# Kernel tuning notes

Measured on AMD Instinct MI355X. Metric: run time of the kernel, lower is better.

Reference implementation:

```python
import jax, jax.numpy as jnp
import numpy as np

N = 50000      # nodes
H = 128        # hidden_size
RBF = 20       # edge_embedding_size
E_CHE = 400000 # chemical edges
E_VDW = 200000 # van-der-Waals edges


def _prelu(x, a):
    return jnp.where(x > 0, x, a * x)


def _mlp(x, w1, b1, a1, w2, b2, a2):
    # Linear -> PReLU -> Linear -> PReLU (PaiNN message / filter MLP)
    h = _prelu(x @ w1 + b1, a1)
    return _prelu(h @ w2 + b2, a2)


def setup_inputs() -> dict:
    key = jax.random.key(0)
    ks = list(jax.random.split(key, 64))
    it = iter(ks)
    d = {}
    d['node_scalar'] = jax.random.normal(next(it), (N, H), jnp.float32)
    d['node_vector'] = jax.random.normal(next(it), (N, 3, H), jnp.float32)
    for pfx, E in (('che', E_CHE), ('vdw', E_VDW)):
        d[pfx + '_edge'] = jax.random.randint(next(it), (E, 2), 0, N)
        d[pfx + '_edge_diff'] = jax.random.normal(next(it), (E, 3), jnp.float32)
        d[pfx + '_edge_dist'] = jax.random.uniform(next(it), (E,), jnp.float32) + 0.5  # strictly positive
        d[pfx + '_rbf_dist'] = jax.random.normal(next(it), (E, RBF), jnp.float32)
    # four 2-layer MLPs with per-layer PReLU scalar slope (torch default init 0.25)
    def mlp_params(pfx, din):
        s1 = 1.0 / np.sqrt(din)
        s2 = 1.0 / np.sqrt(H)
        d[pfx + '_w1'] = jax.random.uniform(next(it), (din, H), jnp.float32, -s1, s1)
        d[pfx + '_b1'] = jax.random.uniform(next(it), (H,), jnp.float32, -s1, s1)
        d[pfx + '_a1'] = jnp.asarray(0.25, jnp.float32)
        d[pfx + '_w2'] = jax.random.uniform(next(it), (H, 3 * H), jnp.float32, -s2, s2)
        d[pfx + '_b2'] = jax.random.uniform(next(it), (3 * H,), jnp.float32, -s2, s2)
        d[pfx + '_a2'] = jnp.asarray(0.25, jnp.float32)
    mlp_params('che_s', H)    # che scalar message MLP
    mlp_params('che_f', RBF)  # che filter layer
    mlp_params('vdw_s', H)
    mlp_params('vdw_f', RBF)
    return d


def _branch(node_scalar, node_vector, edge, edge_diff, edge_dist, rbf, sp, fp):
    # sp/fp: 6-tuples of MLP params. edge[:,1]=source gather, edge[:,0]=dest scatter.
    scalar_out = _mlp(node_scalar, *sp)          # [N, 3H]
    filter_w = _mlp(rbf, *fp)                    # [E, 3H]
    filter_out = scalar_out[edge[:, 1]] * filter_w  # gather + gate
    gate_vector, message_scalar, gate_edge = jnp.split(filter_out, 3, axis=1)
    state_vector = node_vector[edge[:, 1]] * gate_vector[:, None, :]        # [E,3,H]
    unit = edge_diff / edge_dist[:, None]                                    # [E,3]
    edge_vector = unit[:, :, None] * gate_edge[:, None, :]                   # [E,3,H]
    message_vector = state_vector + edge_vector
    res_scalar = jax.ops.segment_sum(message_scalar, edge[:, 0], num_segments=N)
    res_vector = jax.ops.segment_sum(message_vector, edge[:, 0], num_segments=N)
    return res_scalar, res_vector


def reference(node_scalar, node_vector,
              che_edge, che_edge_diff, che_edge_dist, che_rbf_dist,
              vdw_edge, vdw_edge_diff, vdw_edge_dist, vdw_rbf_dist,
              che_s_w1, che_s_b1, che_s_a1, che_s_w2, che_s_b2, che_s_a2,
              che_f_w1, che_f_b1, che_f_a1, che_f_w2, che_f_b2, che_f_a2,
              vdw_s_w1, vdw_s_b1, vdw_s_a1, vdw_s_w2, vdw_s_b2, vdw_s_a2,
              vdw_f_w1, vdw_f_b1, vdw_f_a1, vdw_f_w2, vdw_f_b2, vdw_f_a2):
    che_sp = (che_s_w1, che_s_b1, che_s_a1, che_s_w2, che_s_b2, che_s_a2)
    che_fp = (che_f_w1, che_f_b1, che_f_a1, che_f_w2, che_f_b2, che_f_a2)
    vdw_sp = (vdw_s_w1, vdw_s_b1, vdw_s_a1, vdw_s_w2, vdw_s_b2, vdw_s_a2)
    vdw_fp = (vdw_f_w1, vdw_f_b1, vdw_f_a1, vdw_f_w2, vdw_f_b2, vdw_f_a2)
    che_rs, che_rv = _branch(node_scalar, node_vector, che_edge, che_edge_diff,
                             che_edge_dist, che_rbf_dist, che_sp, che_fp)
    vdw_rs, vdw_rv = _branch(node_scalar, node_vector, vdw_edge, vdw_edge_diff,
                             vdw_edge_dist, vdw_rbf_dist, vdw_sp, vdw_fp)
    return (node_scalar + che_rs + vdw_rs, node_vector + che_rv + vdw_rv)
```

## Files before the change

### kernel.cpp

```cpp
#include <hip/hip_runtime.h>
#include <hip/hip_bf16.h>

typedef float f32x4 __attribute__((ext_vector_type(4)));
typedef short bf16x8 __attribute__((ext_vector_type(8)));

#define HD 128
#define TILE 32
#define SCAN_TILE 2048

__device__ __forceinline__ float prelu_f(float x, float a) {
  return x > 0.f ? x : a * x;
}

__device__ __forceinline__ unsigned short f2bf(float x) {
  __hip_bfloat16 h = __float2bfloat16(x);
  return *reinterpret_cast<unsigned short*>(&h);
}
__device__ __forceinline__ float bf2f(unsigned short u) {
  union { unsigned u; float f; } a; a.u = ((unsigned)u) << 16;
  return a.f;
}
__device__ __forceinline__ f32x4 bf4_to_f32(ushort4 u) {
  f32x4 r; r[0] = bf2f(u.x); r[1] = bf2f(u.y); r[2] = bf2f(u.z); r[3] = bf2f(u.w);
  return r;
}

__global__ __launch_bounds__(256) void init_conv_kernel(
    const f32x4* __restrict__ ns, const f32x4* __restrict__ nv,
    f32x4* __restrict__ out, ushort4* __restrict__ ns_bf, ushort4* __restrict__ nv_bf,
    int n_ns4, int n_nv4)
{
  int total = n_ns4 + n_nv4;
  for (int i = blockIdx.x * 256 + threadIdx.x; i < total; i += gridDim.x * 256) {
    f32x4 v = (i < n_ns4) ? ns[i] : nv[i - n_ns4];
    out[i] = v;
    ushort4 o;
    o.x = f2bf(v[0]); o.y = f2bf(v[1]); o.z = f2bf(v[2]); o.w = f2bf(v[3]);
    if (i < n_ns4) ns_bf[i] = o; else nv_bf[i - n_ns4] = o;
  }
}

__global__ __launch_bounds__(256) void tconv_kernel(
    const float* __restrict__ src, unsigned short* __restrict__ dst)
{
  int idx = blockIdx.x * 256 + threadIdx.x;
  if (idx < 384 * 128) {
    int c = idx >> 7, k = idx & 127;
    dst[idx] = f2bf(src[(size_t)k * 384 + c]);
  }
}

__global__ __launch_bounds__(256) void tconv_w1e_kernel(
    const float* __restrict__ src, unsigned short* __restrict__ dst)
{
  int idx = blockIdx.x * 256 + threadIdx.x;
  if (idx < 128 * 32) {
    int c = idx >> 5, k = idx & 31;
    dst[idx] = (k < 20) ? f2bf(src[(size_t)k * 128 + c]) : (unsigned short)0;
  }
}

__global__ __launch_bounds__(256) void tconv_w1n_kernel(
    const float* __restrict__ src, unsigned short* __restrict__ dst)
{
  int idx = blockIdx.x * 256 + threadIdx.x;
  if (idx < 128 * 128) {
    int c = idx >> 7, k = idx & 127;
    dst[idx] = f2bf(src[(size_t)k * 128 + c]);
  }
}

__global__ __launch_bounds__(256) void node_mlp_mfma(
    const unsigned short* __restrict__ Abf,
    const unsigned short* __restrict__ w1t,
    const float* __restrict__ b1, const float* __restrict__ a1p,
    const unsigned short* __restrict__ w2t,
    const float* __restrict__ b2, const float* __restrict__ a2p,
    unsigned short* __restrict__ out,
    int M)
{
  __shared__ __attribute__((aligned(16))) unsigned short A_lds[64 * HD];
  __shared__ __attribute__((aligned(16))) unsigned short h_lds[64 * HD];
  const int t = threadIdx.x;
  const int wvid = t >> 6, lane = t & 63, l15 = lane & 15, l4 = lane >> 4;
  const int m0 = blockIdx.x * 64;
  const float a1 = a1p[0], a2 = a2p[0];

  for (int idx = t; idx < 64 * HD / 8; idx += 256) {
    int row = idx >> 4, seg = (idx & 15) * 8;
    bf16x8 v = 0;
    if (m0 + row < M) v = *(const bf16x8*)&Abf[(size_t)(m0 + row) * HD + seg];
    *(bf16x8*)&A_lds[row * HD + (seg ^ ((row & 7) << 3))] = v;
  }
  __syncthreads();

  {
    bf16x8 Bf[2][4];
    #pragma unroll
    for (int nf = 0; nf < 2; nf++)
      #pragma unroll
      for (int ks = 0; ks < 4; ks++) {
        int col = wvid * 32 + nf * 16 + l15;
        Bf[nf][ks] = *(const bf16x8*)&w1t[(size_t)col * 128 + ks * 32 + l4 * 8];
      }
    f32x4 D[4][2];
    #pragma unroll
    for (int mi = 0; mi < 4; mi++)
      #pragma unroll
      for (int nf = 0; nf < 2; nf++)
        #pragma unroll
        for (int cc = 0; cc < 4; cc++) D[mi][nf][cc] = 0.f;

    #pragma unroll
    for (int mi = 0; mi < 4; mi++)
      #pragma unroll
      for (int ks = 0; ks < 4; ks++) {
        int row = mi * 16 + l15;
        bf16x8 Af = *(const bf16x8*)&A_lds[row * HD + ((ks * 32 + l4 * 8) ^ ((row & 7) << 3))];
        D[mi][0] = __builtin_amdgcn_mfma_f32_16x16x32_bf16(Af, Bf[0][ks], D[mi][0], 0, 0, 0);
        D[mi][1] = __builtin_amdgcn_mfma_f32_16x16x32_bf16(Af, Bf[1][ks], D[mi][1], 0, 0, 0);
      }

    float b1v0 = b1[wvid * 32 + l15];
    float b1v1 = b1[wvid * 32 + 16 + l15];
    #pragma unroll
    for (int mi = 0; mi < 4; mi++)
      #pragma unroll
      for (int nf = 0; nf < 2; nf++)
        #pragma unroll
        for (int r4 = 0; r4 < 4; r4++) {
          int row = mi * 16 + l4 * 4 + r4;
          int col = wvid * 32 + nf * 16 + l15;
          h_lds[row * HD + (col ^ ((row & 7) << 3))] =
              f2bf(prelu_f(D[mi][nf][r4] + (nf ? b1v1 : b1v0), a1));
        }
  }
  __syncthreads();

  for (int m = 0; m < 3; m++) {
    bf16x8 Bf[2][4];
    #pragma unroll
    for (int nf = 0; nf < 2; nf++)
      #pragma unroll
      for (int ks = 0; ks < 4; ks++) {
        int col = m * 128 + wvid * 32 + nf * 16 + l15;
        Bf[nf][ks] = *(const bf16x8*)&w2t[(size_t)col * 128 + ks * 32 + l4 * 8];
      }
    f32x4 D[4][2];
    #pragma unroll
    for (int mi = 0; mi < 4; mi++)
      #pragma unroll
      for (int nf = 0; nf < 2; nf++)
        #pragma unroll
        for (int cc = 0; cc < 4; cc++) D[mi][nf][cc] = 0.f;

    #pragma unroll
    for (int mi = 0; mi < 4; mi++)
      #pragma unroll
      for (int ks = 0; ks < 4; ks++) {
        int row = mi * 16 + l15;
        bf16x8 Af = *(const bf16x8*)&h_lds[row * HD + ((ks * 32 + l4 * 8) ^ ((row & 7) << 3))];
        D[mi][0] = __builtin_amdgcn_mfma_f32_16x16x32_bf16(Af, Bf[0][ks], D[mi][0], 0, 0, 0);
        D[mi][1] = __builtin_amdgcn_mfma_f32_16x16x32_bf16(Af, Bf[1][ks], D[mi][1], 0, 0, 0);
      }

    float b2v0 = b2[m * 128 + wvid * 32 + l15];
    float b2v1 = b2[m * 128 + wvid * 32 + 16 + l15];
    #pragma unroll
    for (int mi = 0; mi < 4; mi++)
      #pragma unroll
      for (int nf = 0; nf < 2; nf++)
        #pragma unroll
        for (int r4 = 0; r4 < 4; r4++) {
          int row = mi * 16 + l4 * 4 + r4;
          if (m0 + row < M) {
            int col = m * 128 + wvid * 32 + nf * 16 + l15;
            out[(size_t)(m0 + row) * 384 + col] =
                f2bf(prelu_f(D[mi][nf][r4] + (nf ? b2v1 : b2v0), a2));
          }
        }
  }
}

__global__ __launch_bounds__(256) void zero_int_kernel(int* __restrict__ p, int n) {
  int i = blockIdx.x * 256 + threadIdx.x;
  if (i < n) p[i] = 0;
}

__global__ __launch_bounds__(256) void hist_kernel(const int* __restrict__ edge, int* __restrict__ counts, int E) {
  int e = blockIdx.x * 256 + threadIdx.x;
  if (e < E) atomicAdd(&counts[edge[(size_t)e * 2]], 1);
}

__global__ __launch_bounds__(256) void scan_partial_kernel(
    const int* __restrict__ counts, int* __restrict__ partials, int n)
{
  const int b = blockIdx.x, t = threadIdx.x;
  const int base = b * SCAN_TILE + t * 8;
  int s = 0;
  #pragma unroll
  for (int i = 0; i < 8; i++) {
    int idx = base + i;
    if (idx < n) s += counts[idx];
  }
  __shared__ int sums[256];
  sums[t] = s;
  __syncthreads();
  for (int o = 128; o > 0; o >>= 1) {
    if (t < o) sums[t] += sums[t + o];
    __syncthreads();
  }
  if (t == 0) partials[b] = sums[0];
}

__global__ __launch_bounds__(256) void scan_partials_kernel(int* __restrict__ partials, int nb)
{
  __shared__ int s[256];
  const int t = threadIdx.x;
  s[t] = (t < nb) ? partials[t] : 0;
  __syncthreads();
  for (int o = 1; o < 256; o <<= 1) {
    int v = s[t];
    int u = (t >= o) ? s[t - o] : 0;
    __syncthreads();
    s[t] = v + u;
    __syncthreads();
  }
  if (t < nb) partials[t] = (t == 0) ? 0 : s[t - 1];
}

__global__ __launch_bounds__(256) void scan_write_kernel(
    const int* __restrict__ counts, const int* __restrict__ partials,
    int* __restrict__ offsets, int* __restrict__ cursor, int n, int E)
{
  const int b = blockIdx.x, t = threadIdx.x;
  const int base = b * SCAN_TILE + t * 8;
  int vals[8];
  int s = 0;
  #pragma unroll
  for (int i = 0; i < 8; i++) {
    int idx = base + i;
    vals[i] = (idx < n) ? counts[idx] : 0;
    s += vals[i];
  }
  __shared__ int sums[256];
  sums[t] = s;
  __syncthreads();
  for (int o = 1; o < 256; o <<= 1) {
    int v = sums[t];
    int u = (t >= o) ? sums[t - o] : 0;
    __syncthreads();
    sums[t] = v + u;
    __syncthreads();
  }
  int run = partials[b] + ((t == 0) ? 0 : sums[t - 1]);
  #pragma unroll
  for (int i = 0; i < 8; i++) {
    int idx = base + i;
    if (idx < n) {
      offsets[idx] = run;
      cursor[idx] = run;
      run += vals[i];
    }
  }
  if (b == 0 && t == 0) offsets[n] = E;
}

__global__ __launch_bounds__(256) void scatter_ids_kernel(
    const int* __restrict__ edge, int* __restrict__ cursor, int* __restrict__ edge_list, int E)
{
  int e = blockIdx.x * 256 + threadIdx.x;
  if (e < E) {
    int d = edge[(size_t)e * 2];
    int p = atomicAdd(&cursor[d], 1);
    edge_list[p] = e;
  }
}

__global__ __launch_bounds__(256) void permute_edge_kernel(
    const int* __restrict__ edge_list,
    const int* __restrict__ edge, const float* __restrict__ diff,
    const float* __restrict__ dist, const float* __restrict__ rbf,
    int* __restrict__ src_s, int* __restrict__ dst_s,
    float4* __restrict__ unit_s, unsigned short* __restrict__ rbf_b,
    int E)
{
  int p = blockIdx.x * 256 + threadIdx.x;
  if (p >= E) return;
  int e = edge_list[p];
  src_s[p] = edge[(size_t)e * 2 + 1];
  dst_s[p] = edge[(size_t)e * 2 + 0];
  float inv = 1.f / dist[e];
  float4 u;
  u.x = diff[(size_t)e * 3 + 0] * inv;
  u.y = diff[(size_t)e * 3 + 1] * inv;
  u.z = diff[(size_t)e * 3 + 2] * inv;
  u.w = 0.f;
  unit_s[p] = u;
  ushort4* ro = (ushort4*)(rbf_b + (size_t)p * 32);
  const float* rr = &rbf[(size_t)e * 20];
  #pragma unroll
  for (int i = 0; i < 5; i++) {
    ushort4 o;
    o.x = f2bf(rr[4 * i + 0]); o.y = f2bf(rr[4 * i + 1]);
    o.z = f2bf(rr[4 * i + 2]); o.w = f2bf(rr[4 * i + 3]);
    ro[i] = o;
  }
  ushort4 z; z.x = 0; z.y = 0; z.z = 0; z.w = 0;
  ro[5] = z; ro[6] = z; ro[7] = z;
}

__global__ __launch_bounds__(256, 4) void edge_mfma_reduce_kernel(
    const unsigned short* __restrict__ so,
    const unsigned short* __restrict__ nv,
    const int*   __restrict__ src_s,
    const int*   __restrict__ dst_s,
    const float4* __restrict__ unit_s,
    const unsigned short* __restrict__ rbf_b,
    const int*   __restrict__ offsets,
    const unsigned short* __restrict__ w1t,
    const float* __restrict__ b1, const float* __restrict__ a1p,
    const unsigned short* __restrict__ w2t,
    const float* __restrict__ b2, const float* __restrict__ a2p,
    float* __restrict__ out,
    int N, int E)
{
  __shared__ __attribute__((aligned(16))) unsigned short A1_lds[TILE * 40];
  __shared__ __attribute__((aligned(16))) unsigned short h_lds[TILE * HD];
  __shared__ __attribute__((aligned(16))) unsigned short P_lds[3][TILE * HD];
  __shared__ int src_l[TILE];
  __shared__ float unit_l[TILE][3];
  __shared__ int run_rs[TILE + 1], run_node[TILE], run_flag[TILE];
  __shared__ int nd_s;

  const int t = threadIdx.x;
  const int tx = t & 31, ty = t >> 5;
  const int c4 = tx * 4;
  const int wvid = t >> 6, lane = t & 63, l15 = lane & 15, l4 = lane >> 4;
  const int pblk = blockIdx.x * TILE;
  const int nrows = min(TILE, E - pblk);
  const float a1 = a1p[0], a2 = a2p[0];

  if (t < 64) {
    int d = -1, s = 0;
    float ux = 0.f, uy = 0.f, uz = 0.f;
    if (t < nrows) {
      s = src_s[pblk + t];
      d = dst_s[pblk + t];
      float4 u = unit_s[pblk + t];
      ux = u.x; uy = u.y; uz = u.z;
    }
    if (t < TILE) {
      src_l[t] = s;
      unit_l[t][0] = ux; unit_l[t][1] = uy; unit_l[t][2] = uz;
    }
    int dprev = __shfl_up(d, 1);
    bool flag = (t < nrows) && (t == 0 || d != dprev);
    unsigned long long mask = __ballot(flag ? 1 : 0);
    if (flag) {
      int j = __popcll(mask & ((1ull << t) - 1ull));
      run_rs[j] = t;
      run_node[j] = d;
      unsigned long long rest = (t == 63) ? 0ull : (mask >> (t + 1));
      int re = rest ? (t + 1 + (__ffsll((long long)rest) - 1)) : nrows;
      int interior = 1;
      if (t == 0 && offsets[d] != pblk) interior = 0;
      if (re == nrows && offsets[d + 1] != pblk + nrows) interior = 0;
      run_flag[j] = interior;
    }
    if (t == 0) {
      int nd = __popcll(mask);
      nd_s = nd;
      run_rs[nd] = nrows;
    }
  }

  if (t < TILE * 4) {
    const bf16x8* rb = (const bf16x8*)(rbf_b + (size_t)pblk * 32);
    int row = t >> 2, seg = (t & 3) * 8;
    *(bf16x8*)&A1_lds[row * 40 + seg] = rb[t];
  }
  __syncthreads();

  {
    bf16x8 B1[2];
    B1[0] = *(const bf16x8*)&w1t[(size_t)(wvid * 32 + l15) * 32 + l4 * 8];
    B1[1] = *(const bf16x8*)&w1t[(size_t)(wvid * 32 + 16 + l15) * 32 + l4 * 8];
    f32x4 D1[2][2];
    #pragma unroll
    for (int mi = 0; mi < 2; mi++)
      #pragma unroll
      for (int nf = 0; nf < 2; nf++)
        #pragma unroll
        for (int cc = 0; cc < 4; cc++) D1[mi][nf][cc] = 0.f;

    #pragma unroll
    for (int mi = 0; mi < 2; mi++) {
      bf16x8 Af = *(const bf16x8*)&A1_lds[(mi * 16 + l15) * 40 + l4 * 8];
      D1[mi][0] = __builtin_amdgcn_mfma_f32_16x16x32_bf16(Af, B1[0], D1[mi][0], 0, 0, 0);
      D1[mi][1] = __builtin_amdgcn_mfma_f32_16x16x32_bf16(Af, B1[1], D1[mi][1], 0, 0, 0);
    }

    float b1v0 = b1[wvid * 32 + l15];
    float b1v1 = b1[wvid * 32 + 16 + l15];
    #pragma unroll
    for (int mi = 0; mi < 2; mi++)
      #pragma unroll
      for (int nf = 0; nf < 2; nf++)
        #pragma unroll
        for (int r4 = 0; r4 < 4; r4++) {
          int row = mi * 16 + l4 * 4 + r4;
          int col = wvid * 32 + nf * 16 + l15;
          h_lds[row * HD + (col ^ ((row & 7) << 3))] =
              f2bf(prelu_f(D1[mi][nf][r4] + (nf ? b1v1 : b1v0), a1));
        }
  }
  __syncthreads();

  for (int m = 0; m < 3; m++) {
    bf16x8 Bf[2][4];
    #pragma unroll
    for (int nf = 0; nf < 2; nf++)
      #pragma unroll
      for (int ks = 0; ks < 4; ks++) {
        int col = m * 128 + wvid * 32 + nf * 16 + l15;
        Bf[nf][ks] = *(const bf16x8*)&w2t[(size_t)col * 128 + ks * 32 + l4 * 8];
      }
    f32x4 D[2][2];
    #pragma unroll
    for (int mi = 0; mi < 2; mi++)
      #pragma unroll
      for (int nf = 0; nf < 2; nf++)
        #pragma unroll
        for (int cc = 0; cc < 4; cc++) D[mi][nf][cc] = 0.f;

    #pragma unroll
    for (int mi = 0; mi < 2; mi++)
      #pragma unroll
      for (int ks = 0; ks < 4; ks++) {
        int row = mi * 16 + l15;
        bf16x8 Af = *(const bf16x8*)&h_lds[row * HD + ((ks * 32 + l4 * 8) ^ ((row & 7) << 3))];
        D[mi][0] = __builtin_amdgcn_mfma_f32_16x16x32_bf16(Af, Bf[0][ks], D[mi][0], 0, 0, 0);
        D[mi][1] = __builtin_amdgcn_mfma_f32_16x16x32_bf16(Af, Bf[1][ks], D[mi][1], 0, 0, 0);
      }

    float b2v0 = b2[m * 128 + wvid * 32 + l15];
    float b2v1 = b2[m * 128 + wvid * 32 + 16 + l15];
    #pragma unroll
    for (int mi = 0; mi < 2; mi++)
      #pragma unroll
      for (int nf = 0; nf < 2; nf++)
        #pragma unroll
        for (int r4 = 0; r4 < 4; r4++) {
          int row = mi * 16 + l4 * 4 + r4;
          int col = wvid * 32 + nf * 16 + l15;
          float v = prelu_f(D[mi][nf][r4] + (nf ? b2v1 : b2v0), a2);
          P_lds[m][row * HD + (col ^ ((row & 7) << 3))] = f2bf(v);
        }
  }
  __syncthreads();

  #pragma unroll
  for (int rr = 0; rr < 4; rr++) {
    const int r = ty * 4 + rr;
    const int src = src_l[r];
    const int sc = c4 ^ ((r & 7) << 3);
    f32x4 gvp = bf4_to_f32(*(const ushort4*)&P_lds[0][r * HD + sc]);
    f32x4 msp = bf4_to_f32(*(const ushort4*)&P_lds[1][r * HD + sc]);
    f32x4 gep = bf4_to_f32(*(const ushort4*)&P_lds[2][r * HD + sc]);
    const size_t sb = (size_t)src * 384;
    f32x4 s0 = bf4_to_f32(*(const ushort4*)&so[sb + c4]);
    f32x4 s1 = bf4_to_f32(*(const ushort4*)&so[sb + HD + c4]);
    f32x4 s2 = bf4_to_f32(*(const ushort4*)&so[sb + 2 * HD + c4]);
    f32x4 v0 = bf4_to_f32(*(const ushort4*)&nv[sb + c4]);
    f32x4 v1 = bf4_to_f32(*(const ushort4*)&nv[sb + HD + c4]);
    f32x4 v2 = bf4_to_f32(*(const ushort4*)&nv[sb + 2 * HD + c4]);
    const float u0 = unit_l[r][0], u1 = unit_l[r][1], u2 = unit_l[r][2];
    ushort4 msw, m0w, m1w, m2w;
    #pragma unroll
    for (int cc = 0; cc < 4; cc++) {
      float gv = gvp[cc] * s0[cc];
      float ms = msp[cc] * s1[cc];
      float ge = gep[cc] * s2[cc];
      float mv0 = v0[cc] * gv + u0 * ge;
      float mv1 = v1[cc] * gv + u1 * ge;
      float mv2 = v2[cc] * gv + u2 * ge;
      ((unsigned short*)&msw)[cc] = f2bf(ms);
      ((unsigned short*)&m0w)[cc] = f2bf(mv0);
      ((unsigned short*)&m1w)[cc] = f2bf(mv1);
      ((unsigned short*)&m2w)[cc] = f2bf(mv2);
    }
    *(ushort4*)&h_lds[r * HD + sc]    = msw;
    *(ushort4*)&P_lds[0][r * HD + sc] = m0w;
    *(ushort4*)&P_lds[1][r * HD + sc] = m1w;
    *(ushort4*)&P_lds[2][r * HD + sc] = m2w;
  }
  __syncthreads();

  {
    const int pl = t >> 6;
    const int c2 = (t & 63) * 2;
    const unsigned short* region = (pl == 0) ? h_lds : &P_lds[pl - 1][0];
    float* out_v = out + (size_t)N * HD;
    const int nd = nd_s;
    for (int j = 0; j < nd; j++) {
      const int rs = run_rs[j], re = run_rs[j + 1];
      const int n = run_node[j];
      float a0 = 0.f, a1v = 0.f;
      for (int r = rs; r < re; r++) {
        int ad = r * HD + (((c2 & ~3) ^ ((r & 7) << 3)) | (c2 & 3));
        unsigned int u = *(const unsigned int*)&region[ad];
        a0  += bf2f((unsigned short)(u & 0xffffu));
        a1v += bf2f((unsigned short)(u >> 16));
      }
      float* dstp = (pl == 0) ? (out + (size_t)n * HD + c2)
                              : (out_v + (size_t)n * 384 + (size_t)(pl - 1) * HD + c2);
      if (run_flag[j]) {
        float2 cur = *(float2*)dstp;
        cur.x += a0; cur.y += a1v;
        *(float2*)dstp = cur;
      } else {
        atomicAdd(dstp, a0);
        atomicAdd(dstp + 1, a1v);
      }
    }
  }
}

extern "C" void kernel_launch(void* const* d_in, const int* in_sizes, int n_in,
                              void* d_out, int out_size, void* d_ws, size_t ws_size,
                              hipStream_t stream)
{
  const float* node_scalar = (const float*)d_in[0];
  const float* node_vector = (const float*)d_in[1];
  const int*   che_edge = (const int*)d_in[2];
  const float* che_diff = (const float*)d_in[3];
  const float* che_dist = (const float*)d_in[4];
  const float* che_rbf  = (const float*)d_in[5];
  const int*   vdw_edge = (const int*)d_in[6];
  const float* vdw_diff = (const float*)d_in[7];
  const float* vdw_dist = (const float*)d_in[8];
  const float* vdw_rbf  = (const float*)d_in[9];
  const float* mlp_p[24];
  for (int i = 0; i < 24; i++) mlp_p[i] = (const float*)d_in[10 + i];

  const int N = in_sizes[0] / HD;
  const int E_che = in_sizes[4];
  const int E_vdw = in_sizes[8];
  const int E_max = E_che > E_vdw ? E_che : E_vdw;
  const int E_pad = (E_max + 63) & ~63;
  const int nb_scan = (N + SCAN_TILE - 1) / SCAN_TILE;

  char* wp = (char*)d_ws;
  size_t off = 0;
  unsigned short* so_bf = (unsigned short*)(wp + off); off += (size_t)N * 384 * 2;
  unsigned short* nv_bf = (unsigned short*)(wp + off); off += (size_t)N * 384 * 2;
  unsigned short* ns_bf = (unsigned short*)(wp + off); off += (size_t)N * 128 * 2;
  int* counts     = (int*)(wp + off);   off += (size_t)N * 4;
  int* cursor     = (int*)(wp + off);   off += (size_t)N * 4;
  int* offsets    = (int*)(wp + off);   off += (size_t)(N + 1) * 4;
  int* partials   = (int*)(wp + off);   off += 256 * 4;
  off = (off + 255) & ~(size_t)255;
  int* edge_list  = (int*)(wp + off);   off += (size_t)E_max * 4;
  int* src_s      = (int*)(wp + off);   off += (size_t)E_max * 4;
  int* dst_s      = (int*)(wp + off);   off += (size_t)E_max * 4;
  off = (off + 255) & ~(size_t)255;
  float4* unit_s  = (float4*)(wp + off); off += (size_t)E_max * 16;
  unsigned short* rbf_b = (unsigned short*)(wp + off); off += (size_t)E_pad * 64;
  off = (off + 255) & ~(size_t)255;
  unsigned short* w2t_sche = (unsigned short*)(wp + off); off += 384 * 128 * 2;
  unsigned short* w2t_fche = (unsigned short*)(wp + off); off += 384 * 128 * 2;
  unsigned short* w2t_svdw = (unsigned short*)(wp + off); off += 384 * 128 * 2;
  unsigned short* w2t_fvdw = (unsigned short*)(wp + off); off += 384 * 128 * 2;
  unsigned short* w1t_nche = (unsigned short*)(wp + off); off += 128 * 128 * 2;
  unsigned short* w1t_nvdw = (unsigned short*)(wp + off); off += 128 * 128 * 2;
  unsigned short* w1t_eche = (unsigned short*)(wp + off); off += 128 * 32 * 2;
  unsigned short* w1t_evdw = (unsigned short*)(wp + off); off += 128 * 32 * 2;

  const int n_ns4 = N * HD / 4;
  const int n_nv4 = N * 3 * HD / 4;
  init_conv_kernel<<<2048, 256, 0, stream>>>(
      (const f32x4*)node_scalar, (const f32x4*)node_vector, (f32x4*)d_out,
      (ushort4*)ns_bf, (ushort4*)nv_bf, n_ns4, n_nv4);

  tconv_kernel<<<192, 256, 0, stream>>>(mlp_p[3],  w2t_sche);
  tconv_kernel<<<192, 256, 0, stream>>>(mlp_p[9],  w2t_fche);
  tconv_kernel<<<192, 256, 0, stream>>>(mlp_p[15], w2t_svdw);
  tconv_kernel<<<192, 256, 0, stream>>>(mlp_p[21], w2t_fvdw);
  tconv_w1n_kernel<<<64, 256, 0, stream>>>(mlp_p[0],  w1t_nche);
  tconv_w1n_kernel<<<64, 256, 0, stream>>>(mlp_p[12], w1t_nvdw);
  tconv_w1e_kernel<<<16, 256, 0, stream>>>(mlp_p[6],  w1t_eche);
  tconv_w1e_kernel<<<16, 256, 0, stream>>>(mlp_p[18], w1t_evdw);

  for (int br = 0; br < 2; br++) {
    const int*   edge = br == 0 ? che_edge : vdw_edge;
    const float* diff = br == 0 ? che_diff : vdw_diff;
    const float* dist = br == 0 ? che_dist : vdw_dist;
    const float* rbf  = br == 0 ? che_rbf  : vdw_rbf;
    const int    E    = br == 0 ? E_che : E_vdw;
    const float* const* sp = &mlp_p[br == 0 ? 0 : 12];
    const float* const* fp = &mlp_p[br == 0 ? 6 : 18];
    const unsigned short* w2t_s = br == 0 ? w2t_sche : w2t_svdw;
    const unsigned short* w2t_f = br == 0 ? w2t_fche : w2t_fvdw;
    const unsigned short* w1t_n = br == 0 ? w1t_nche : w1t_nvdw;
    const unsigned short* w1t_e = br == 0 ? w1t_eche : w1t_evdw;

    node_mlp_mfma<<<(N + 63) / 64, 256, 0, stream>>>(
        ns_bf, w1t_n, sp[1], sp[2], w2t_s, sp[4], sp[5], so_bf, N);

    zero_int_kernel<<<(N + 255) / 256, 256, 0, stream>>>(counts, N);
    hist_kernel<<<(E + 255) / 256, 256, 0, stream>>>(edge, counts, E);
    scan_partial_kernel<<<nb_scan, 256, 0, stream>>>(counts, partials, N);
    scan_partials_kernel<<<1, 256, 0, stream>>>(partials, nb_scan);
    scan_write_kernel<<<nb_scan, 256, 0, stream>>>(counts, partials, offsets, cursor, N, E);
    scatter_ids_kernel<<<(E + 255) / 256, 256, 0, stream>>>(edge, cursor, edge_list, E);
    permute_edge_kernel<<<(E + 255) / 256, 256, 0, stream>>>(
        edge_list, edge, diff, dist, rbf, src_s, dst_s, unit_s, rbf_b, E);

    edge_mfma_reduce_kernel<<<(E + TILE - 1) / TILE, 256, 0, stream>>>(
        so_bf, nv_bf, src_s, dst_s, unit_s, rbf_b, offsets,
        w1t_e, fp[1], fp[2], w2t_f, fp[4], fp[5],
        (float*)d_out, N, E);
  }
}
```

Measured before the change: 650.2 us.

## Batch CSR build for both branches and prefetch source gathers early

Merges the weight transpose kernels into one launch and builds the destination-sorted edge structures for both branches in a single pass of combined histogram, scan, scatter and permute kernels. This cuts the number of launches and lets the small preprocessing kernels fill more of the device. The edge kernel now issues the gathers of source-node scalar and vector rows into registers at kernel entry, so their latency overlaps the MLP work. The cost is higher register pressure in the edge kernel, which may lower occupancy, and larger workspace buffers.

```diff
diff --git a/kernel.cpp b/kernel.cpp
--- a/kernel.cpp
+++ b/kernel.cpp
@@ -40,33 +40,37 @@
   }
 }
 
-__global__ __launch_bounds__(256) void tconv_kernel(
-    const float* __restrict__ src, unsigned short* __restrict__ dst)
+__global__ __launch_bounds__(256) void weights_prep_kernel(
+    const float* __restrict__ w2s_che, const float* __restrict__ w2f_che,
+    const float* __restrict__ w2s_vdw, const float* __restrict__ w2f_vdw,
+    const float* __restrict__ w1n_che, const float* __restrict__ w1n_vdw,
+    const float* __restrict__ w1e_che, const float* __restrict__ w1e_vdw,
+    unsigned short* __restrict__ d_w2t_sche, unsigned short* __restrict__ d_w2t_fche,
+    unsigned short* __restrict__ d_w2t_svdw, unsigned short* __restrict__ d_w2t_fvdw,
+    unsigned short* __restrict__ d_w1t_nche, unsigned short* __restrict__ d_w1t_nvdw,
+    unsigned short* __restrict__ d_w1t_eche, unsigned short* __restrict__ d_w1t_evdw)
 {
   int idx = blockIdx.x * 256 + threadIdx.x;
-  if (idx < 384 * 128) {
-    int c = idx >> 7, k = idx & 127;
-    dst[idx] = f2bf(src[(size_t)k * 384 + c]);
-  }
-}
-
-__global__ __launch_bounds__(256) void tconv_w1e_kernel(
-    const float* __restrict__ src, unsigned short* __restrict__ dst)
-{
-  int idx = blockIdx.x * 256 + threadIdx.x;
-  if (idx < 128 * 32) {
-    int c = idx >> 5, k = idx & 31;
-    dst[idx] = (k < 20) ? f2bf(src[(size_t)k * 128 + c]) : (unsigned short)0;
-  }
-}
-
-__global__ __launch_bounds__(256) void tconv_w1n_kernel(
-    const float* __restrict__ src, unsigned short* __restrict__ dst)
-{
-  int idx = blockIdx.x * 256 + threadIdx.x;
-  if (idx < 128 * 128) {
-    int c = idx >> 7, k = idx & 127;
-    dst[idx] = f2bf(src[(size_t)k * 128 + c]);
+  if (idx < 4 * 49152) {
+    int which = idx / 49152, rem = idx % 49152;
+    int c = rem >> 7, k = rem & 127;
+    const float* s = which == 0 ? w2s_che : which == 1 ? w2f_che : which == 2 ? w2s_vdw : w2f_vdw;
+    unsigned short* d = which == 0 ? d_w2t_sche : which == 1 ? d_w2t_fche : which == 2 ? d_w2t_svdw : d_w2t_fvdw;
+    d[rem] = f2bf(s[(size_t)k * 384 + c]);
+  } else if (idx < 4 * 49152 + 2 * 16384) {
+    int rem2 = idx - 4 * 49152;
+    int which = rem2 / 16384, rem = rem2 % 16384;
+    int c = rem >> 7, k = rem & 127;
+    const float* s = which ? w1n_vdw : w1n_che;
+    unsigned short* d = which ? d_w1t_nvdw : d_w1t_nche;
+    d[rem] = f2bf(s[(size_t)k * 128 + c]);
+  } else if (idx < 4 * 49152 + 2 * 16384 + 2 * 4096) {
+    int rem2 = idx - 4 * 49152 - 2 * 16384;
+    int which = rem2 / 4096, rem = rem2 % 4096;
+    int c = rem >> 5, k = rem & 31;
+    const float* s = which ? w1e_vdw : w1e_che;
+    unsigned short* d = which ? d_w1t_evdw : d_w1t_eche;
+    d[rem] = (k < 20) ? f2bf(s[(size_t)k * 128 + c]) : (unsigned short)0;
   }
 }
 
@@ -187,21 +191,31 @@
   if (i < n) p[i] = 0;
 }
 
-__global__ __launch_bounds__(256) void hist_kernel(const int* __restrict__ edge, int* __restrict__ counts, int E) {
-  int e = blockIdx.x * 256 + threadIdx.x;
-  if (e < E) atomicAdd(&counts[edge[(size_t)e * 2]], 1);
-}
-
-__global__ __launch_bounds__(256) void scan_partial_kernel(
-    const int* __restrict__ counts, int* __restrict__ partials, int n)
+__global__ __launch_bounds__(256) void hist2_kernel(
+    const int* __restrict__ edge_che, const int* __restrict__ edge_vdw,
+    int* __restrict__ counts, int N, int E_che, int E_vdw)
+{
+  int g = blockIdx.x * 256 + threadIdx.x;
+  if (g < E_che) {
+    atomicAdd(&counts[edge_che[(size_t)g * 2]], 1);
+  } else {
+    int e2 = g - E_che;
+    if (e2 < E_vdw) atomicAdd(&counts[N + edge_vdw[(size_t)e2 * 2]], 1);
+  }
+}
+
+__global__ __launch_bounds__(256) void scan_partial2_kernel(
+    const int* __restrict__ counts, int* __restrict__ partials, int n, int nb)
 {
   const int b = blockIdx.x, t = threadIdx.x;
-  const int base = b * SCAN_TILE + t * 8;
+  const int br = b >= nb, lb = b - br * nb;
+  const int* cnt = counts + (size_t)br * n;
+  const int base = lb * SCAN_TILE + t * 8;
   int s = 0;
   #pragma unroll
   for (int i = 0; i < 8; i++) {
     int idx = base + i;
-    if (idx < n) s += counts[idx];
+    if (idx < n) s += cnt[idx];
   }
   __shared__ int sums[256];
   sums[t] = s;
@@ -213,8 +227,9 @@
   if (t == 0) partials[b] = sums[0];
 }
 
-__global__ __launch_bounds__(256) void scan_partials_kernel(int* __restrict__ partials, int nb)
-{
+__global__ __launch_bounds__(256) void scan_partials2_kernel(int* __restrict__ partials_g, int nb)
+{
+  int* partials = partials_g + blockIdx.x * nb;
   __shared__ int s[256];
   const int t = threadIdx.x;
   s[t] = (t < nb) ? partials[t] : 0;
@@ -229,18 +244,23 @@
   if (t < nb) partials[t] = (t == 0) ? 0 : s[t - 1];
 }
 
-__global__ __launch_bounds__(256) void scan_write_kernel(
+__global__ __launch_bounds__(256) void scan_write2_kernel(
     const int* __restrict__ counts, const int* __restrict__ partials,
-    int* __restrict__ offsets, int* __restrict__ cursor, int n, int E)
+    int* __restrict__ offsets, int* __restrict__ cursor, int n, int nb,
+    int E_che, int E_vdw)
 {
   const int b = blockIdx.x, t = threadIdx.x;
-  const int base = b * SCAN_TILE + t * 8;
+  const int br = b >= nb, lb = b - br * nb;
+  const int* cnt = counts + (size_t)br * n;
+  int* offs = offsets + (size_t)br * (n + 1);
+  int* curs = cursor + (size_t)br * n;
+  const int base = lb * SCAN_TILE + t * 8;
   int vals[8];
   int s = 0;
   #pragma unroll
   for (int i = 0; i < 8; i++) {
     int idx = base + i;
-    vals[i] = (idx < n) ? counts[idx] : 0;
+    vals[i] = (idx < n) ? cnt[idx] : 0;
     s += vals[i];
   }
   __shared__ int sums[256];
@@ -258,36 +278,52 @@
   for (int i = 0; i < 8; i++) {
     int idx = base + i;
     if (idx < n) {
-      offsets[idx] = run;
-      cursor[idx] = run;
+      offs[idx] = run;
+      curs[idx] = run;
       run += vals[i];
     }
   }
-  if (b == 0 && t == 0) offsets[n] = E;
-}
-
-__global__ __launch_bounds__(256) void scatter_ids_kernel(
-    const int* __restrict__ edge, int* __restrict__ cursor, int* __restrict__ edge_list, int E)
-{
-  int e = blockIdx.x * 256 + threadIdx.x;
-  if (e < E) {
-    int d = edge[(size_t)e * 2];
+  if (lb == 0 && t == 0) offs[n] = br ? E_vdw : E_che;
+}
+
+__global__ __launch_bounds__(256) void scatter_ids2_kernel(
+    const int* __restrict__ edge_che, const int* __restrict__ edge_vdw,
+    int* __restrict__ cursor, int* __restrict__ edge_list,
+    int N, int E_che, int E_vdw)
+{
+  int g = blockIdx.x * 256 + threadIdx.x;
+  if (g < E_che) {
+    int d = edge_che[(size_t)g * 2];
     int p = atomicAdd(&cursor[d], 1);
-    edge_list[p] = e;
-  }
-}
-
-__global__ __launch_bounds__(256) void permute_edge_kernel(
+    edge_list[p] = g;
+  } else {
+    int e2 = g - E_che;
+    if (e2 < E_vdw) {
+      int d = edge_vdw[(size_t)e2 * 2];
+      int p = atomicAdd(&cursor[N + d], 1);
+      edge_list[E_che + p] = e2;
+    }
+  }
+}
+
+__global__ __launch_bounds__(256) void permute2_kernel(
     const int* __restrict__ edge_list,
-    const int* __restrict__ edge, const float* __restrict__ diff,
-    const float* __restrict__ dist, const float* __restrict__ rbf,
+    const int* __restrict__ edge_che, const float* __restrict__ diff_che,
+    const float* __restrict__ dist_che, const float* __restrict__ rbf_che,
+    const int* __restrict__ edge_vdw, const float* __restrict__ diff_vdw,
+    const float* __restrict__ dist_vdw, const float* __restrict__ rbf_vdw,
     int* __restrict__ src_s, int* __restrict__ dst_s,
     float4* __restrict__ unit_s, unsigned short* __restrict__ rbf_b,
-    int E)
+    int E_che, int E_vdw)
 {
   int p = blockIdx.x * 256 + threadIdx.x;
-  if (p >= E) return;
+  if (p >= E_che + E_vdw) return;
+  int br = p >= E_che;
   int e = edge_list[p];
+  const int* edge = br ? edge_vdw : edge_che;
+  const float* diff = br ? diff_vdw : diff_che;
+  const float* dist = br ? dist_vdw : dist_che;
+  const float* rbf  = br ? rbf_vdw  : rbf_che;
   src_s[p] = edge[(size_t)e * 2 + 1];
   dst_s[p] = edge[(size_t)e * 2 + 0];
   float inv = 1.f / dist[e];
@@ -328,7 +364,6 @@
   __shared__ __attribute__((aligned(16))) unsigned short A1_lds[TILE * 40];
   __shared__ __attribute__((aligned(16))) unsigned short h_lds[TILE * HD];
   __shared__ __attribute__((aligned(16))) unsigned short P_lds[3][TILE * HD];
-  __shared__ int src_l[TILE];
   __shared__ float unit_l[TILE][3];
   __shared__ int run_rs[TILE + 1], run_node[TILE], run_flag[TILE];
   __shared__ int nd_s;
@@ -341,17 +376,29 @@
   const int nrows = min(TILE, E - pblk);
   const float a1 = a1p[0], a2 = a2p[0];
 
+  ushort4 pf_s0[4], pf_s1[4], pf_s2[4], pf_v0[4], pf_v1[4], pf_v2[4];
+  #pragma unroll
+  for (int rr = 0; rr < 4; rr++) {
+    int p = pblk + ty * 4 + rr;
+    int src = (p < E) ? src_s[p] : 0;
+    const size_t sb = (size_t)src * 384;
+    pf_s0[rr] = *(const ushort4*)&so[sb + c4];
+    pf_s1[rr] = *(const ushort4*)&so[sb + HD + c4];
+    pf_s2[rr] = *(const ushort4*)&so[sb + 2 * HD + c4];
+    pf_v0[rr] = *(const ushort4*)&nv[sb + c4];
+    pf_v1[rr] = *(const ushort4*)&nv[sb + HD + c4];
+    pf_v2[rr] = *(const ushort4*)&nv[sb + 2 * HD + c4];
+  }
+
   if (t < 64) {
-    int d = -1, s = 0;
+    int d = -1;
     float ux = 0.f, uy = 0.f, uz = 0.f;
     if (t < nrows) {
-      s = src_s[pblk + t];
       d = dst_s[pblk + t];
       float4 u = unit_s[pblk + t];
       ux = u.x; uy = u.y; uz = u.z;
     }
     if (t < TILE) {
-      src_l[t] = s;
       unit_l[t][0] = ux; unit_l[t][1] = uy; unit_l[t][2] = uz;
     }
     int dprev = __shfl_up(d, 1);
@@ -463,18 +510,16 @@
   #pragma unroll
   for (int rr = 0; rr < 4; rr++) {
     const int r = ty * 4 + rr;
-    const int src = src_l[r];
     const int sc = c4 ^ ((r & 7) << 3);
     f32x4 gvp = bf4_to_f32(*(const ushort4*)&P_lds[0][r * HD + sc]);
     f32x4 msp = bf4_to_f32(*(const ushort4*)&P_lds[1][r * HD + sc]);
     f32x4 gep = bf4_to_f32(*(const ushort4*)&P_lds[2][r * HD + sc]);
-    const size_t sb = (size_t)src * 384;
-    f32x4 s0 = bf4_to_f32(*(const ushort4*)&so[sb + c4]);
-    f32x4 s1 = bf4_to_f32(*(const ushort4*)&so[sb + HD + c4]);
-    f32x4 s2 = bf4_to_f32(*(const ushort4*)&so[sb + 2 * HD + c4]);
-    f32x4 v0 = bf4_to_f32(*(const ushort4*)&nv[sb + c4]);
-    f32x4 v1 = bf4_to_f32(*(const ushort4*)&nv[sb + HD + c4]);
-    f32x4 v2 = bf4_to_f32(*(const ushort4*)&nv[sb + 2 * HD + c4]);
+    f32x4 s0 = bf4_to_f32(pf_s0[rr]);
+    f32x4 s1 = bf4_to_f32(pf_s1[rr]);
+    f32x4 s2 = bf4_to_f32(pf_s2[rr]);
+    f32x4 v0 = bf4_to_f32(pf_v0[rr]);
+    f32x4 v1 = bf4_to_f32(pf_v1[rr]);
+    f32x4 v2 = bf4_to_f32(pf_v2[rr]);
     const float u0 = unit_l[r][0], u1 = unit_l[r][1], u2 = unit_l[r][2];
     ushort4 msw, m0w, m1w, m2w;
     #pragma unroll
@@ -547,8 +592,7 @@
   const int N = in_sizes[0] / HD;
   const int E_che = in_sizes[4];
   const int E_vdw = in_sizes[8];
-  const int E_max = E_che > E_vdw ? E_che : E_vdw;
-  const int E_pad = (E_max + 63) & ~63;
+  const int E_sum = E_che + E_vdw;
   const int nb_scan = (N + SCAN_TILE - 1) / SCAN_TILE;
 
   char* wp = (char*)d_ws;
@@ -556,17 +600,17 @@
   unsigned short* so_bf = (unsigned short*)(wp + off); off += (size_t)N * 384 * 2;
   unsigned short* nv_bf = (unsigned short*)(wp + off); off += (size_t)N * 384 * 2;
   unsigned short* ns_bf = (unsigned short*)(wp + off); off += (size_t)N * 128 * 2;
-  int* counts     = (int*)(wp + off);   off += (size_t)N * 4;
-  int* cursor     = (int*)(wp + off);   off += (size_t)N * 4;
-  int* offsets    = (int*)(wp + off);   off += (size_t)(N + 1) * 4;
-  int* partials   = (int*)(wp + off);   off += 256 * 4;
+  int* counts     = (int*)(wp + off);   off += (size_t)2 * N * 4;
+  int* cursor     = (int*)(wp + off);   off += (size_t)2 * N * 4;
+  int* offsets    = (int*)(wp + off);   off += (size_t)2 * (N + 1) * 4;
+  int* partials   = (int*)(wp + off);   off += 512 * 4;
   off = (off + 255) & ~(size_t)255;
-  int* edge_list  = (int*)(wp + off);   off += (size_t)E_max * 4;
-  int* src_s      = (int*)(wp + off);   off += (size_t)E_max * 4;
-  int* dst_s      = (int*)(wp + off);   off += (size_t)E_max * 4;
+  int* edge_list  = (int*)(wp + off);   off += (size_t)E_sum * 4;
+  int* src_s      = (int*)(wp + off);   off += (size_t)E_sum * 4;
+  int* dst_s      = (int*)(wp + off);   off += (size_t)E_sum * 4;
   off = (off + 255) & ~(size_t)255;
-  float4* unit_s  = (float4*)(wp + off); off += (size_t)E_max * 16;
-  unsigned short* rbf_b = (unsigned short*)(wp + off); off += (size_t)E_pad * 64;
+  float4* unit_s  = (float4*)(wp + off); off += (size_t)E_sum * 16;
+  unsigned short* rbf_b = (unsigned short*)(wp + off); off += (size_t)E_sum * 64;
   off = (off + 255) & ~(size_t)255;
   unsigned short* w2t_sche = (unsigned short*)(wp + off); off += 384 * 128 * 2;
   unsigned short* w2t_fche = (unsigned short*)(wp + off); off += 384 * 128 * 2;
@@ -583,21 +627,30 @@
       (const f32x4*)node_scalar, (const f32x4*)node_vector, (f32x4*)d_out,
       (ushort4*)ns_bf, (ushort4*)nv_bf, n_ns4, n_nv4);
 
-  tconv_kernel<<<192, 256, 0, stream>>>(mlp_p[3],  w2t_sche);
-  tconv_kernel<<<192, 256, 0, stream>>>(mlp_p[9],  w2t_fche);
-  tconv_kernel<<<192, 256, 0, stream>>>(mlp_p[15], w2t_svdw);
-  tconv_kernel<<<192, 256, 0, stream>>>(mlp_p[21], w2t_fvdw);
-  tconv_w1n_kernel<<<64, 256, 0, stream>>>(mlp_p[0],  w1t_nche);
-  tconv_w1n_kernel<<<64, 256, 0, stream>>>(mlp_p[12], w1t_nvdw);
-  tconv_w1e_kernel<<<16, 256, 0, stream>>>(mlp_p[6],  w1t_eche);
-  tconv_w1e_kernel<<<16, 256, 0, stream>>>(mlp_p[18], w1t_evdw);
+  weights_prep_kernel<<<928, 256, 0, stream>>>(
+      mlp_p[3], mlp_p[9], mlp_p[15], mlp_p[21],
+      mlp_p[0], mlp_p[12], mlp_p[6], mlp_p[18],
+      w2t_sche, w2t_fche, w2t_svdw, w2t_fvdw,
+      w1t_nche, w1t_nvdw, w1t_eche, w1t_evdw);
+
+  zero_int_kernel<<<(2 * N + 255) / 256, 256, 0, stream>>>(counts, 2 * N);
+  hist2_kernel<<<(E_sum + 255) / 256, 256, 0, stream>>>(
+      che_edge, vdw_edge, counts, N, E_che, E_vdw);
+  scan_partial2_kernel<<<2 * nb_scan, 256, 0, stream>>>(counts, partials, N, nb_scan);
+  scan_partials2_kernel<<<2, 256, 0, stream>>>(partials, nb_scan);
+  scan_write2_kernel<<<2 * nb_scan, 256, 0, stream>>>(
+      counts, partials, offsets, cursor, N, nb_scan, E_che, E_vdw);
+  scatter_ids2_kernel<<<(E_sum + 255) / 256, 256, 0, stream>>>(
+      che_edge, vdw_edge, cursor, edge_list, N, E_che, E_vdw);
+  permute2_kernel<<<(E_sum + 255) / 256, 256, 0, stream>>>(
+      edge_list,
+      che_edge, che_diff, che_dist, che_rbf,
+      vdw_edge, vdw_diff, vdw_dist, vdw_rbf,
+      src_s, dst_s, unit_s, rbf_b, E_che, E_vdw);
 
   for (int br = 0; br < 2; br++) {
-    const int*   edge = br == 0 ? che_edge : vdw_edge;
-    const float* diff = br == 0 ? che_diff : vdw_diff;
-    const float* dist = br == 0 ? che_dist : vdw_dist;
-    const float* rbf  = br == 0 ? che_rbf  : vdw_rbf;
-    const int    E    = br == 0 ? E_che : E_vdw;
+    const int E = br == 0 ? E_che : E_vdw;
+    const int base = br == 0 ? 0 : E_che;
     const float* const* sp = &mlp_p[br == 0 ? 0 : 12];
     const float* const* fp = &mlp_p[br == 0 ? 6 : 18];
     const unsigned short* w2t_s = br == 0 ? w2t_sche : w2t_svdw;
@@ -608,17 +661,10 @@
     node_mlp_mfma<<<(N + 63) / 64, 256, 0, stream>>>(
         ns_bf, w1t_n, sp[1], sp[2], w2t_s, sp[4], sp[5], so_bf, N);
 
-    zero_int_kernel<<<(N + 255) / 256, 256, 0, stream>>>(counts, N);
-    hist_kernel<<<(E + 255) / 256, 256, 0, stream>>>(edge, counts, E);
-    scan_partial_kernel<<<nb_scan, 256, 0, stream>>>(counts, partials, N);
-    scan_partials_kernel<<<1, 256, 0, stream>>>(partials, nb_scan);
-    scan_write_kernel<<<nb_scan, 256, 0, stream>>>(counts, partials, offsets, cursor, N, E);
-    scatter_ids_kernel<<<(E + 255) / 256, 256, 0, stream>>>(edge, cursor, edge_list, E);
-    permute_edge_kernel<<<(E + 255) / 256, 256, 0, stream>>>(
-        edge_list, edge, diff, dist, rbf, src_s, dst_s, unit_s, rbf_b, E);
-
     edge_mfma_reduce_kernel<<<(E + TILE - 1) / TILE, 256, 0, stream>>>(
-        so_bf, nv_bf, src_s, dst_s, unit_s, rbf_b, offsets,
+        so_bf, nv_bf,
+        src_s + base, dst_s + base, unit_s + base, rbf_b + (size_t)base * 32,
+        offsets + (size_t)br * (N + 1),
         w1t_e, fp[1], fp[2], w2t_f, fp[4], fp[5],
         (float*)d_out, N, E);
   }
```

Result: slower. 719.3 us (+10.6%).
